# Kernel optimization log

Measured on AMD Instinct MI355X. Metric: run time of the kernel, lower is better.

## Reference

```python
import jax, jax.numpy as jnp
import numpy as np

ALPHA = 0.2        # LeakyReLU negative slope used in standard GAT
NEG_INF = -9e15    # mask fill value from the canonical pyGAT implementation


def _gat_layer(x, adj_mask, W, a1, a2, concat):
    """One GAT attention head.
    x: [B,N,Din], adj_mask: [B,N,N] bool, W: [Din,Dout], a1/a2: [Dout].
    """
    Wh = jnp.einsum('bnd,df->bnf', x, W)               # [B,N,Dout]
    f1 = jnp.einsum('bnf,f->bn', Wh, a1)               # source scores
    f2 = jnp.einsum('bnf,f->bn', Wh, a2)               # target scores
    e = jax.nn.leaky_relu(f1[:, :, None] + f2[:, None, :], ALPHA)  # [B,N,N]
    e = jnp.where(adj_mask, e, jnp.float32(NEG_INF))
    attn = jax.nn.softmax(e, axis=-1)                  # masked row-softmax
    out = jnp.einsum('bnm,bmf->bnf', attn, Wh)         # neighbor aggregation
    return jax.nn.elu(out) if concat else out


def setup_inputs() -> dict:
    key = jax.random.key(0)
    ks = jax.random.split(key, 8)
    B, N, Din, Dout, H = 32, 512, 768, 256, 8
    x = jax.random.normal(ks[0], (B, N, Din), jnp.float32)
    adj = jax.random.randint(ks[1], (B, N, N), 0, 2, jnp.int32)  # {0,1} adjacency
    W0 = jax.random.normal(ks[2], (H, Din, Dout), jnp.float32) * (1.0 / np.sqrt(Din))
    a1_0 = jax.random.normal(ks[3], (H, Dout), jnp.float32) * 0.1
    a2_0 = jax.random.normal(ks[4], (H, Dout), jnp.float32) * 0.1
    Wo = jax.random.normal(ks[5], (Dout, Dout), jnp.float32) * (1.0 / np.sqrt(Dout))
    a1_o = jax.random.normal(ks[6], (Dout,), jnp.float32) * 0.1
    a2_o = jax.random.normal(ks[7], (Dout,), jnp.float32) * 0.1
    return dict(x=x, adj=adj, W0=W0, a1_0=a1_0, a2_0=a2_0,
                Wo=Wo, a1_o=a1_o, a2_o=a2_o)


def reference(x, adj, W0, a1_0, a2_0, Wo, a1_o, a2_o):
    mask = adj > 0
    # multi-head layer: vmap over heads replaces the Python head loop
    heads = jax.vmap(lambda W, a1, a2: _gat_layer(x, mask, W, a1, a2, True))(
        W0, a1_0, a2_0)                                # [H,B,N,Dout]
    h = heads.mean(axis=0)                             # cat+unsqueeze+mean(dim=1)
    # dropout is identity in eval mode (p effectively 0 for the baseline)
    out = _gat_layer(h, mask, Wo, a1_o, a2_o, False)   # gat_out, concat=False
    return jax.nn.relu(out)                            # [B,N,Dout]
```

## Files before the change

### kernel.cpp

```cpp
#include <hip/hip_runtime.h>
#include <hip/hip_bf16.h>
#include <stdint.h>

typedef __bf16 bf16;
typedef short short8 __attribute__((ext_vector_type(8)));
typedef float f32x4 __attribute__((ext_vector_type(4)));

#define LOG2E 1.4426950408889634f

union V16 { uint4 u; short8 s; bf16 h[8]; };
union U8  { ushort4 s; bf16 h[4]; };

typedef const __attribute__((address_space(1))) void* gp_t;
typedef __attribute__((address_space(3))) void* lp_t;
__device__ __forceinline__ void gld16(const bf16* g, bf16* l) {
  __builtin_amdgcn_global_load_lds((gp_t)g, (lp_t)l, 16, 0, 0);
}

__global__ __launch_bounds__(256) void k_zero(float4* __restrict__ p, int n4) {
  int i = blockIdx.x * 256 + threadIdx.x;
  if (i < n4) p[i] = {0.f, 0.f, 0.f, 0.f};
}

__global__ __launch_bounds__(256) void k_cvt(const float* __restrict__ src,
                                             bf16* __restrict__ dst, long long n) {
  long long i = ((long long)blockIdx.x * 256 + threadIdx.x) * 8;
  if (i >= n) return;
  float4 a = *(const float4*)(src + i);
  float4 b = *(const float4*)(src + i + 4);
  U8 w0, w1;
  w0.h[0] = (bf16)a.x; w0.h[1] = (bf16)a.y; w0.h[2] = (bf16)a.z; w0.h[3] = (bf16)a.w;
  w1.h[0] = (bf16)b.x; w1.h[1] = (bf16)b.y; w1.h[2] = (bf16)b.z; w1.h[3] = (bf16)b.w;
  *(ushort4*)(dst + i)     = w0.s;
  *(ushort4*)(dst + i + 4) = w1.s;
}

__global__ __launch_bounds__(256) void k_maskpack(const int* __restrict__ adj,
                                                  unsigned long long* __restrict__ mask) {
  int wid = blockIdx.x * 4 + (threadIdx.x >> 6);
  int lane = threadIdx.x & 63;
  int a = adj[(long long)wid * 64 + lane];
  unsigned long long m = __ballot(a > 0);
  if (lane == 0) mask[wid] = m;
}

__global__ __launch_bounds__(256) void k_transpose(const float* __restrict__ src,
                                                   bf16* __restrict__ dst, int R, int C) {
  __shared__ float t[32][33];
  int c0 = blockIdx.x * 32, r0 = blockIdx.y * 32;
  src += (long long)blockIdx.z * R * C;
  dst += (long long)blockIdx.z * R * C;
  int tx = threadIdx.x & 31, ty = threadIdx.x >> 5;
  for (int rr = ty; rr < 32; rr += 8)
    t[rr][tx] = src[(long long)(r0 + rr) * C + (c0 + tx)];
  __syncthreads();
  for (int cc = ty; cc < 32; cc += 8)
    dst[(long long)(c0 + cc) * R + (r0 + tx)] = (bf16)t[tx][cc];
}

__global__ __launch_bounds__(256) void k_gemm(const bf16* __restrict__ A,
                                              const bf16* __restrict__ WT,
                                              bf16* __restrict__ outT, int K,
                                              const float* __restrict__ a1,
                                              const float* __restrict__ a2,
                                              int aStride,
                                              float* __restrict__ f1out,
                                              float* __restrict__ f2out) {
  __shared__ bf16 As[128 * 32];
  __shared__ bf16 Bs[128 * 32];
  const int nb = blockIdx.x, mb = blockIdx.y, h = blockIdx.z;
  const int tid = threadIdx.x, wave = tid >> 6, lane = tid & 63;
  const int lrow = lane & 15, quad = lane >> 4;
  const long long mbase = (long long)mb * 128;
  const int nbase = nb * 128;
  const bf16* W = WT + (long long)h * 256 * K;
  const int wm = (wave >> 1) * 64, wn = (wave & 1) * 64;
  const int srow = wave * 16 + (lane >> 2);
  const int skoff = (lane & 3) * 8;
  const bf16* ag0 = A + (mbase + srow) * K + skoff;
  const bf16* ag1 = ag0 + 64 * K;
  const bf16* bg0 = W + (long long)(nbase + srow) * K + skoff;
  const bf16* bg1 = bg0 + 64 * K;
  bf16* lA0 = As + wave * 16 * 32;
  bf16* lA1 = As + (64 + wave * 16) * 32;
  bf16* lB0 = Bs + wave * 16 * 32;
  bf16* lB1 = Bs + (64 + wave * 16) * 32;
  f32x4 acc[4][4];
#pragma unroll
  for (int i = 0; i < 4; i++)
#pragma unroll
    for (int j = 0; j < 4; j++) acc[i][j] = {0.f, 0.f, 0.f, 0.f};
  for (int k0 = 0; k0 < K; k0 += 32) {
    __syncthreads();
    gld16(ag0 + k0, lA0);
    gld16(ag1 + k0, lA1);
    gld16(bg0 + k0, lB0);
    gld16(bg1 + k0, lB1);
    __syncthreads();
    V16 af[4], bfx[4];
#pragma unroll
    for (int mi = 0; mi < 4; mi++)
      af[mi].u = *(const uint4*)(As + (wm + mi * 16 + lrow) * 32 + quad * 8);
#pragma unroll
    for (int ni = 0; ni < 4; ni++)
      bfx[ni].u = *(const uint4*)(Bs + (wn + ni * 16 + lrow) * 32 + quad * 8);
#pragma unroll
    for (int mi = 0; mi < 4; mi++)
#pragma unroll
      for (int ni = 0; ni < 4; ni++)
        acc[mi][ni] = __builtin_amdgcn_mfma_f32_16x16x32_bf16(af[mi].s, bfx[ni].s, acc[mi][ni], 0, 0, 0);
  }
#pragma unroll
  for (int mi = 0; mi < 4; mi++) {
    long long m0 = mbase + wm + mi * 16 + quad * 4;
    int bbi = (int)(m0 >> 9);
    int jj = (int)(m0 & 511);
    int js = jj >> 5, qp = (jj >> 3) & 3, eo = jj & 7;
    long long rowbase = (long long)(h * 32 + bbi) * 131072 +
                        (long long)js * 512 + (qp * 16 + lrow) * 8 + eo;
#pragma unroll
    for (int ni = 0; ni < 4; ni++) {
      int ft = ((nbase + wn) >> 4) + ni;
      U8 w;
#pragma unroll
      for (int r = 0; r < 4; r++) w.h[r] = (bf16)acc[mi][ni][r];
      *(ushort4*)(outT + rowbase + (long long)ft * 8192) = w.s;
    }
  }
  float av1[4], av2[4];
#pragma unroll
  for (int ni = 0; ni < 4; ni++) {
    int f = nbase + wn + ni * 16 + lrow;
    av1[ni] = a1[h * aStride + f];
    av2[ni] = a2[h * aStride + f];
  }
#pragma unroll
  for (int mi = 0; mi < 4; mi++) {
#pragma unroll
    for (int r = 0; r < 4; r++) {
      float s1 = 0.f, s2 = 0.f;
#pragma unroll
      for (int ni = 0; ni < 4; ni++) {
        s1 = __builtin_fmaf(acc[mi][ni][r], av1[ni], s1);
        s2 = __builtin_fmaf(acc[mi][ni][r], av2[ni], s2);
      }
#pragma unroll
      for (int off = 1; off < 16; off <<= 1) {
        s1 += __shfl_xor(s1, off);
        s2 += __shfl_xor(s2, off);
      }
      if (lrow == 0) {
        long long m0 = mbase + wm + mi * 16 + quad * 4 + r;
        atomicAdd(&f1out[(long long)h * 16384 + m0], s1);
        atomicAdd(&f2out[(long long)h * 16384 + m0], s2);
      }
    }
  }
}

__global__ __launch_bounds__(256) void k_passA(const float* __restrict__ f1p,
                                               const float* __restrict__ f2p,
                                               const unsigned long long* __restrict__ mask,
                                               float* __restrict__ cc) {
  const int hb = blockIdx.x, bb = hb & 31;
  const int wave = threadIdx.x >> 6, lane = threadIdx.x & 63;
  const int i = blockIdx.y * 4 + wave;
  const float* f2 = f2p + hb * 512;
  float4 va = *(const float4*)(f2 + lane * 8);
  float4 vb = *(const float4*)(f2 + lane * 8 + 4);
  float vj[8] = {va.x, va.y, va.z, va.w, vb.x, vb.y, vb.z, vb.w};
  unsigned int mb = ((const unsigned char*)(mask + ((long long)bb * 512 + i) * 8))[lane];
  float f1 = f1p[hb * 512 + i];
  float m = -INFINITY;
#pragma unroll
  for (int t = 0; t < 8; t++)
    if ((mb >> t) & 1) m = fmaxf(m, vj[t]);
#pragma unroll
  for (int off = 32; off; off >>= 1) m = fmaxf(m, __shfl_xor(m, off));
  float s = f1 + m;
  float M2 = LOG2E * fmaxf(s, 0.2f * s);
  float d = 0.f;
#pragma unroll
  for (int t = 0; t < 8; t++) {
    float e0 = f1 + vj[t];
    float e = fmaxf(e0, 0.2f * e0);
    float p = exp2f(__builtin_fmaf(LOG2E, e, -M2));
    d += ((mb >> t) & 1) ? p : 0.f;
  }
#pragma unroll
  for (int off = 32; off; off >>= 1) d += __shfl_xor(d, off);
  if (lane == 0) {
    float cv = M2 + log2f(d);
    if (!isfinite(M2) || !(d > 0.f)) cv = INFINITY;
    cc[hb * 512 + i] = cv;
  }
}

__device__ __forceinline__ int pchunk(int row, int c) {
  return row * 512 + (((c + 3 * row) & 63) << 3);
}

template <int NSPLIT, int NHB, int ROWS, int MODE>
__global__ __launch_bounds__(256) void k_pv(const bf16* __restrict__ WhT,
                                            const float* __restrict__ f1p,
                                            const float* __restrict__ cc,
                                            const float* __restrict__ f2p,
                                            const unsigned long long* __restrict__ mask,
                                            void* __restrict__ out0,
                                            void* __restrict__ out1) {
  constexpr int TPR = 256 / ROWS;
  constexpr int NT  = 64 / TPR;
  constexpr int MI  = ROWS / 16;
  constexpr int RB  = 32 * (512 / ROWS);
  constexpr int CPT = 256 / TPR;
  __shared__ union { bf16 P[ROWS * 512]; float hs[ROWS * 264]; } sh;
  __shared__ unsigned char ms[ROWS * 64];
  const int id = blockIdx.x;
  const int hp = id / RB;
  const int rid = id % RB;
  const int bb = rid & 31, it = rid >> 5;
  const int ibase = it * ROWS;
  const int tid = threadIdx.x, wave = tid >> 6, lane = tid & 63;
  const int lrow = lane & 15, quad = lane >> 4;
  const int pi = tid / TPR;
  const int pj = tid % TPR;
  {
    const uint4* msrc = (const uint4*)(mask + ((long long)bb * 512 + ibase) * 8);
    if (tid < ROWS * 4) ((uint4*)ms)[tid] = msrc[tid];
  }
  __syncthreads();
  unsigned long long mreg = 0;
#pragma unroll
  for (int t = 0; t < NT; t++)
    mreg |= (unsigned long long)ms[pi * 64 + pj + t * TPR] << (t * 8);
  f32x4 hacc[MI][4];
#pragma unroll
  for (int i = 0; i < MI; i++)
#pragma unroll
    for (int j = 0; j < 4; j++) hacc[i][j] = {0.f, 0.f, 0.f, 0.f};

  auto buildP = [&](int h) {
    const int hb = h * 32 + bb;
    const float f1v = f1p[hb * 512 + ibase + pi];
    const float cv  = cc[hb * 512 + ibase + pi];
    const float Ac = __builtin_fmaf(LOG2E, f1v, -cv);
    const float Bc = __builtin_fmaf(0.2f * LOG2E, f1v, -cv);
    const float* f2 = f2p + hb * 512;
#pragma unroll
    for (int t = 0; t < NT; t++) {
      const int ch = pj + t * TPR;
      const int j0 = ch * 8;
      float4 u0 = *(const float4*)(f2 + j0);
      float4 u1 = *(const float4*)(f2 + j0 + 4);
      float fj[8] = {u0.x, u0.y, u0.z, u0.w, u1.x, u1.y, u1.z, u1.w};
      unsigned int mb = (unsigned int)(mreg >> (t * 8)) & 0xff;
      V16 pk;
#pragma unroll
      for (int u = 0; u < 8; u++) {
        float e = fmaxf(__builtin_fmaf(LOG2E, fj[u], Ac),
                        __builtin_fmaf(0.2f * LOG2E, fj[u], Bc));
        float p = ((mb >> u) & 1) ? exp2f(e) : 0.f;
        pk.h[u] = (bf16)p;
      }
      *(uint4*)(sh.P + pchunk(pi, ch)) = pk.u;
    }
  };

#pragma unroll 1
  for (int hh = 0; hh < NHB; hh++) {
    const int h = hp * NHB + hh;
    const int hb = h * 32 + bb;
    __syncthreads();
    buildP(h);
    __syncthreads();
    const bf16* wfb = WhT + (long long)hb * 131072 + (long long)wave * 32768 + lane * 8;
    f32x4 acc[MI][4];
#pragma unroll
    for (int i = 0; i < MI; i++)
#pragma unroll
      for (int j = 0; j < 4; j++) acc[i][j] = {0.f, 0.f, 0.f, 0.f};
#pragma unroll
    for (int js = 0; js < 16; js++) {
      V16 af[MI], bfr[4];
#pragma unroll
      for (int mi = 0; mi < MI; mi++)
        af[mi].u = *(const uint4*)(sh.P + pchunk(mi * 16 + lrow, js * 4 + quad));
#pragma unroll
      for (int ni = 0; ni < 4; ni++)
        bfr[ni].u = *(const uint4*)(wfb + ni * 8192 + js * 512);
#pragma unroll
      for (int ni = 0; ni < 4; ni++)
#pragma unroll
        for (int mi = 0; mi < MI; mi++)
          acc[mi][ni] = __builtin_amdgcn_mfma_f32_16x16x32_bf16(af[mi].s, bfr[ni].s, acc[mi][ni], 0, 0, 0);
    }
#pragma unroll
    for (int mi = 0; mi < MI; mi++)
#pragma unroll
      for (int ni = 0; ni < 4; ni++)
#pragma unroll
        for (int r = 0; r < 4; r++) {
          float v = acc[mi][ni][r];
          hacc[mi][ni][r] += (MODE == 1) ? v
                           : (v > 0.f ? v : (exp2f(v * LOG2E) - 1.f));
        }
  }
  __syncthreads();
#pragma unroll
  for (int mi = 0; mi < MI; mi++)
#pragma unroll
    for (int ni = 0; ni < 4; ni++) {
      int f = wave * 64 + ni * 16 + lrow;
#pragma unroll
      for (int r = 0; r < 4; r++) {
        int row = mi * 16 + quad * 4 + r;
        sh.hs[row * 264 + f] = hacc[mi][ni][r];
      }
    }
  __syncthreads();
  const int fb = pj * CPT;
  float* op = (float*)(hp ? out1 : out0) +
              (((long long)bb * 512) + ibase + pi) * 256 + fb;
#pragma unroll
  for (int c0 = 0; c0 < CPT; c0 += 4) {
    float4 w;
    w.x = sh.hs[pi * 264 + fb + c0 + 0];
    w.y = sh.hs[pi * 264 + fb + c0 + 1];
    w.z = sh.hs[pi * 264 + fb + c0 + 2];
    w.w = sh.hs[pi * 264 + fb + c0 + 3];
    if (MODE == 1) {
      w.x = fmaxf(w.x, 0.f); w.y = fmaxf(w.y, 0.f);
      w.z = fmaxf(w.z, 0.f); w.w = fmaxf(w.w, 0.f);
    }
    *(float4*)(op + c0) = w;
  }
}

__global__ __launch_bounds__(256) void k_fin(const float* __restrict__ a,
                                             const float* __restrict__ b,
                                             bf16* __restrict__ dst) {
  long long i = ((long long)blockIdx.x * 256 + threadIdx.x) * 4;
  float4 x = *(const float4*)(a + i);
  float4 y = *(const float4*)(b + i);
  U8 w;
  w.h[0] = (bf16)((x.x + y.x) * 0.125f);
  w.h[1] = (bf16)((x.y + y.y) * 0.125f);
  w.h[2] = (bf16)((x.z + y.z) * 0.125f);
  w.h[3] = (bf16)((x.w + y.w) * 0.125f);
  *(ushort4*)(dst + i) = w.s;
}

extern "C" void kernel_launch(void* const* d_in, const int* in_sizes, int n_in,
                              void* d_out, int out_size, void* d_ws, size_t ws_size,
                              hipStream_t stream) {
  const float* x    = (const float*)d_in[0];
  const int*   adj  = (const int*)d_in[1];
  const float* W0   = (const float*)d_in[2];
  const float* a1_0 = (const float*)d_in[3];
  const float* a2_0 = (const float*)d_in[4];
  const float* Wo   = (const float*)d_in[5];
  const float* a1_o = (const float*)d_in[6];
  const float* a2_o = (const float*)d_in[7];

  char* p = (char*)d_ws;
  auto take = [&](size_t n) { char* r = p; p += (n + 255) & ~(size_t)255; return r; };
  unsigned long long* maskb = (unsigned long long*)take(32ull * 512 * 8 * 8);
  bf16*  xb   = (bf16*)take(32ull * 512 * 768 * 2);
  bf16*  W0T  = (bf16*)take(8ull * 256 * 768 * 2);
  bf16*  WoT  = (bf16*)take(256ull * 256 * 2);
  bf16*  WhT  = (bf16*)take(8ull * 32 * 256 * 512 * 2);
  float* f1p1 = (float*)take(8ull * 32 * 512 * 4);
  float* f2p1 = (float*)take(8ull * 32 * 512 * 4);
  float* f1p2 = (float*)take(32ull * 512 * 4);
  float* f2p2 = (float*)take(32ull * 512 * 4);
  float* c1   = (float*)take(8ull * 32 * 512 * 4);
  float* c2   = (float*)take(32ull * 512 * 4);
  float* pv1  = (float*)take(32ull * 512 * 256 * 4);
  float* pv0  = (float*)xb;
  bf16*  hmid = (bf16*)((char*)xb + 16ull * 1024 * 1024);
  bf16*  Wh2T = WhT;

  k_zero<<<288, 256, 0, stream>>>((float4*)f1p1, 73728);
  k_cvt<<<6144, 256, 0, stream>>>(x, xb, 32ll * 512 * 768);
  k_maskpack<<<32768, 256, 0, stream>>>(adj, maskb);
  k_transpose<<<dim3(8, 24, 8), 256, 0, stream>>>(W0, W0T, 768, 256);
  k_transpose<<<dim3(8, 8, 1), 256, 0, stream>>>(Wo, WoT, 256, 256);
  k_gemm<<<dim3(2, 128, 8), 256, 0, stream>>>(xb, W0T, WhT, 768,
                                              a1_0, a2_0, 256, f1p1, f2p1);
  k_passA<<<dim3(256, 128), 256, 0, stream>>>(f1p1, f2p1, maskb, c1);
  k_pv<2, 4, 32, 0><<<1024, 256, 0, stream>>>(WhT, f1p1, c1, f2p1, maskb, pv0, pv1);
  k_fin<<<4096, 256, 0, stream>>>(pv0, pv1, hmid);
  k_gemm<<<dim3(2, 128, 1), 256, 0, stream>>>(hmid, WoT, Wh2T, 256,
                                              a1_o, a2_o, 0, f1p2, f2p2);
  k_passA<<<dim3(32, 128), 256, 0, stream>>>(f1p2, f2p2, maskb, c2);
  k_pv<1, 1, 16, 1><<<1024, 256, 0, stream>>>(Wh2T, f1p2, c2, f2p2, maskb, d_out, nullptr);
}
```

Before: 405.0 us.

## Fuse softmax row-max/denominator pass into PV kernel and prefetch Wh fragments

```diff
diff --git a/kernel.cpp b/kernel.cpp
--- a/kernel.cpp
+++ b/kernel.cpp
@@ -15,6 +15,13 @@
 typedef __attribute__((address_space(3))) void* lp_t;
 __device__ __forceinline__ void gld16(const bf16* g, bf16* l) {
   __builtin_amdgcn_global_load_lds((gp_t)g, (lp_t)l, 16, 0, 0);
+}
+
+__device__ __forceinline__ void barrier_lds() {
+  __builtin_amdgcn_sched_barrier(0);
+  asm volatile("s_waitcnt lgkmcnt(0)" ::: "memory");
+  __builtin_amdgcn_s_barrier();
+  __builtin_amdgcn_sched_barrier(0);
 }
 
 __global__ __launch_bounds__(256) void k_zero(float4* __restrict__ p, int n4) {
@@ -158,44 +165,6 @@
   }
 }
 
-__global__ __launch_bounds__(256) void k_passA(const float* __restrict__ f1p,
-                                               const float* __restrict__ f2p,
-                                               const unsigned long long* __restrict__ mask,
-                                               float* __restrict__ cc) {
-  const int hb = blockIdx.x, bb = hb & 31;
-  const int wave = threadIdx.x >> 6, lane = threadIdx.x & 63;
-  const int i = blockIdx.y * 4 + wave;
-  const float* f2 = f2p + hb * 512;
-  float4 va = *(const float4*)(f2 + lane * 8);
-  float4 vb = *(const float4*)(f2 + lane * 8 + 4);
-  float vj[8] = {va.x, va.y, va.z, va.w, vb.x, vb.y, vb.z, vb.w};
-  unsigned int mb = ((const unsigned char*)(mask + ((long long)bb * 512 + i) * 8))[lane];
-  float f1 = f1p[hb * 512 + i];
-  float m = -INFINITY;
-#pragma unroll
-  for (int t = 0; t < 8; t++)
-    if ((mb >> t) & 1) m = fmaxf(m, vj[t]);
-#pragma unroll
-  for (int off = 32; off; off >>= 1) m = fmaxf(m, __shfl_xor(m, off));
-  float s = f1 + m;
-  float M2 = LOG2E * fmaxf(s, 0.2f * s);
-  float d = 0.f;
-#pragma unroll
-  for (int t = 0; t < 8; t++) {
-    float e0 = f1 + vj[t];
-    float e = fmaxf(e0, 0.2f * e0);
-    float p = exp2f(__builtin_fmaf(LOG2E, e, -M2));
-    d += ((mb >> t) & 1) ? p : 0.f;
-  }
-#pragma unroll
-  for (int off = 32; off; off >>= 1) d += __shfl_xor(d, off);
-  if (lane == 0) {
-    float cv = M2 + log2f(d);
-    if (!isfinite(M2) || !(d > 0.f)) cv = INFINITY;
-    cc[hb * 512 + i] = cv;
-  }
-}
-
 __device__ __forceinline__ int pchunk(int row, int c) {
   return row * 512 + (((c + 3 * row) & 63) << 3);
 }
@@ -203,7 +172,6 @@
 template <int NSPLIT, int NHB, int ROWS, int MODE>
 __global__ __launch_bounds__(256) void k_pv(const bf16* __restrict__ WhT,
                                             const float* __restrict__ f1p,
-                                            const float* __restrict__ cc,
                                             const float* __restrict__ f2p,
                                             const unsigned long long* __restrict__ mask,
                                             void* __restrict__ out0,
@@ -214,6 +182,7 @@
   constexpr int RB  = 32 * (512 / ROWS);
   constexpr int CPT = 256 / TPR;
   __shared__ union { bf16 P[ROWS * 512]; float hs[ROWS * 264]; } sh;
+  __shared__ float dinvs[ROWS];
   __shared__ unsigned char ms[ROWS * 64];
   const int id = blockIdx.x;
   const int hp = id / RB;
@@ -228,7 +197,7 @@
     const uint4* msrc = (const uint4*)(mask + ((long long)bb * 512 + ibase) * 8);
     if (tid < ROWS * 4) ((uint4*)ms)[tid] = msrc[tid];
   }
-  __syncthreads();
+  barrier_lds();
   unsigned long long mreg = 0;
 #pragma unroll
   for (int t = 0; t < NT; t++)
@@ -241,11 +210,26 @@
 
   auto buildP = [&](int h) {
     const int hb = h * 32 + bb;
-    const float f1v = f1p[hb * 512 + ibase + pi];
-    const float cv  = cc[hb * 512 + ibase + pi];
-    const float Ac = __builtin_fmaf(LOG2E, f1v, -cv);
-    const float Bc = __builtin_fmaf(0.2f * LOG2E, f1v, -cv);
-    const float* f2 = f2p + hb * 512;
+    const float F1L = LOG2E * f1p[hb * 512 + ibase + pi];
+    const float* f2 = f2p + (long long)hb * 512;
+    float mx = -INFINITY;
+#pragma unroll
+    for (int t = 0; t < NT; t++) {
+      const int j0 = (pj + t * TPR) * 8;
+      float4 u0 = *(const float4*)(f2 + j0);
+      float4 u1 = *(const float4*)(f2 + j0 + 4);
+      float fj[8] = {u0.x, u0.y, u0.z, u0.w, u1.x, u1.y, u1.z, u1.w};
+      unsigned int mb = (unsigned int)(mreg >> (t * 8)) & 0xff;
+#pragma unroll
+      for (int u = 0; u < 8; u++) {
+        float a = __builtin_fmaf(LOG2E, fj[u], F1L);
+        float e = fmaxf(a, 0.2f * a);
+        mx = fmaxf(mx, ((mb >> u) & 1) ? e : -INFINITY);
+      }
+    }
+#pragma unroll
+    for (int off = 1; off < TPR; off <<= 1) mx = fmaxf(mx, __shfl_xor(mx, off));
+    float d = 0.f;
 #pragma unroll
     for (int t = 0; t < NT; t++) {
       const int ch = pj + t * TPR;
@@ -257,23 +241,31 @@
       V16 pk;
 #pragma unroll
       for (int u = 0; u < 8; u++) {
-        float e = fmaxf(__builtin_fmaf(LOG2E, fj[u], Ac),
-                        __builtin_fmaf(0.2f * LOG2E, fj[u], Bc));
-        float p = ((mb >> u) & 1) ? exp2f(e) : 0.f;
+        float a = __builtin_fmaf(LOG2E, fj[u], F1L);
+        float e = fmaxf(a, 0.2f * a);
+        float p = ((mb >> u) & 1) ? exp2f(e - mx) : 0.f;
         pk.h[u] = (bf16)p;
+        d += p;
       }
       *(uint4*)(sh.P + pchunk(pi, ch)) = pk.u;
     }
+#pragma unroll
+    for (int off = 1; off < TPR; off <<= 1) d += __shfl_xor(d, off);
+    if (pj == 0) dinvs[pi] = (d > 0.f) ? (1.f / d) : 0.f;
   };
 
 #pragma unroll 1
   for (int hh = 0; hh < NHB; hh++) {
     const int h = hp * NHB + hh;
     const int hb = h * 32 + bb;
-    __syncthreads();
+    const bf16* wfb = WhT + (long long)hb * 131072 + (long long)wave * 32768 + lane * 8;
+    V16 bcur[4], bnxt[4];
+#pragma unroll
+    for (int ni = 0; ni < 4; ni++)
+      bcur[ni].u = *(const uint4*)(wfb + ni * 8192);
+    barrier_lds();
     buildP(h);
-    __syncthreads();
-    const bf16* wfb = WhT + (long long)hb * 131072 + (long long)wave * 32768 + lane * 8;
+    barrier_lds();
     f32x4 acc[MI][4];
 #pragma unroll
     for (int i = 0; i < MI; i++)
@@ -281,26 +273,36 @@
       for (int j = 0; j < 4; j++) acc[i][j] = {0.f, 0.f, 0.f, 0.f};
 #pragma unroll
     for (int js = 0; js < 16; js++) {
-      V16 af[MI], bfr[4];
+      if (js < 15) {
+#pragma unroll
+        for (int ni = 0; ni < 4; ni++)
+          bnxt[ni].u = *(const uint4*)(wfb + ni * 8192 + (js + 1) * 512);
+      }
+      V16 af[MI];
 #pragma unroll
       for (int mi = 0; mi < MI; mi++)
         af[mi].u = *(const uint4*)(sh.P + pchunk(mi * 16 + lrow, js * 4 + quad));
 #pragma unroll
       for (int ni = 0; ni < 4; ni++)
-        bfr[ni].u = *(const uint4*)(wfb + ni * 8192 + js * 512);
+#pragma unroll
+        for (int mi = 0; mi < MI; mi++)
+          acc[mi][ni] = __builtin_amdgcn_mfma_f32_16x16x32_bf16(af[mi].s, bcur[ni].s, acc[mi][ni], 0, 0, 0);
+#pragma unroll
+      for (int ni = 0; ni < 4; ni++) bcur[ni] = bnxt[ni];
+    }
+    float drow[MI][4];
+#pragma unroll
+    for (int mi = 0; mi < MI; mi++)
+#pragma unroll
+      for (int r = 0; r < 4; r++)
+        drow[mi][r] = dinvs[mi * 16 + quad * 4 + r];
+#pragma unroll
+    for (int mi = 0; mi < MI; mi++)
 #pragma unroll
       for (int ni = 0; ni < 4; ni++)
 #pragma unroll
-        for (int mi = 0; mi < MI; mi++)
-          acc[mi][ni] = __builtin_amdgcn_mfma_f32_16x16x32_bf16(af[mi].s, bfr[ni].s, acc[mi][ni], 0, 0, 0);
-    }
-#pragma unroll
-    for (int mi = 0; mi < MI; mi++)
-#pragma unroll
-      for (int ni = 0; ni < 4; ni++)
-#pragma unroll
         for (int r = 0; r < 4; r++) {
-          float v = acc[mi][ni][r];
+          float v = acc[mi][ni][r] * drow[mi][r];
           hacc[mi][ni][r] += (MODE == 1) ? v
                            : (v > 0.f ? v : (exp2f(v * LOG2E) - 1.f));
         }
@@ -373,8 +375,6 @@
   float* f2p1 = (float*)take(8ull * 32 * 512 * 4);
   float* f1p2 = (float*)take(32ull * 512 * 4);
   float* f2p2 = (float*)take(32ull * 512 * 4);
-  float* c1   = (float*)take(8ull * 32 * 512 * 4);
-  float* c2   = (float*)take(32ull * 512 * 4);
   float* pv1  = (float*)take(32ull * 512 * 256 * 4);
   float* pv0  = (float*)xb;
   bf16*  hmid = (bf16*)((char*)xb + 16ull * 1024 * 1024);
@@ -387,11 +387,9 @@
   k_transpose<<<dim3(8, 8, 1), 256, 0, stream>>>(Wo, WoT, 256, 256);
   k_gemm<<<dim3(2, 128, 8), 256, 0, stream>>>(xb, W0T, WhT, 768,
                                               a1_0, a2_0, 256, f1p1, f2p1);
-  k_passA<<<dim3(256, 128), 256, 0, stream>>>(f1p1, f2p1, maskb, c1);
-  k_pv<2, 4, 32, 0><<<1024, 256, 0, stream>>>(WhT, f1p1, c1, f2p1, maskb, pv0, pv1);
+  k_pv<2, 4, 32, 0><<<1024, 256, 0, stream>>>(WhT, f1p1, f2p1, maskb, pv0, pv1);
   k_fin<<<4096, 256, 0, stream>>>(pv0, pv1, hmid);
   k_gemm<<<dim3(2, 128, 1), 256, 0, stream>>>(hmid, WoT, Wh2T, 256,
                                               a1_o, a2_o, 0, f1p2, f2p2);
-  k_passA<<<dim3(32, 128), 256, 0, stream>>>(f1p2, f2p2, maskb, c2);
-  k_pv<1, 1, 16, 1><<<1024, 256, 0, stream>>>(Wh2T, f1p2, c2, f2p2, maskb, d_out, nullptr);
-}
+  k_pv<1, 1, 16, 1><<<1024, 256, 0, stream>>>(Wh2T, f1p2, f2p2, maskb, d_out, nullptr);
+}
```

Result: slower. 511.3 us (+26.2%).
